# Performance work log

Measured on AMD Instinct MI355X. Metric: run time of the kernel, lower is better.

Reference implementation:

```python
import jax, jax.numpy as jnp
import numpy as np

B, S, D = 2, 1024, 1024
H, HD = 16, 64          # n_heads, head_dim (H*HD == D)
E, FF = 8, 2816         # num_experts, moe hidden_dim
TOP_K = 2               # hard-coded torch.topk(scores, 2)
EPS = 1e-5


def rmsnorm(x, w):
    return x * jax.lax.rsqrt(jnp.mean(x * x, axis=-1, keepdims=True) + EPS) * w


def apply_rope(x, cos, sin):
    # x: [B,S,H,HD]; cos/sin: [S,HD//2] -> interleaved rotary (llama style)
    xr, xi = x[..., 0::2], x[..., 1::2]
    c = cos[None, :, None, :]
    s = sin[None, :, None, :]
    out_r = xr * c - xi * s
    out_i = xr * s + xi * c
    return jnp.stack([out_r, out_i], axis=-1).reshape(x.shape)


def setup_inputs() -> dict:
    key = jax.random.key(0)
    ks = jax.random.split(key, 10)
    sc = 0.02
    pos = jnp.arange(S, dtype=jnp.float32)
    inv = 1.0 / (10000.0 ** (jnp.arange(0, HD, 2, dtype=jnp.float32) / HD))
    ang = pos[:, None] * inv[None, :]                       # [S, HD//2]
    return {
        "x": jax.random.normal(ks[0], (B, S, D), jnp.float32),
        "freqs_cos": jnp.cos(ang),
        "freqs_sin": jnp.sin(ang),
        "attn_norm_w": jnp.ones((D,), jnp.float32),
        "wq": jax.random.normal(ks[1], (D, D), jnp.float32) * sc,
        "wk": jax.random.normal(ks[2], (D, D), jnp.float32) * sc,
        "wv": jax.random.normal(ks[3], (D, D), jnp.float32) * sc,
        "wo": jax.random.normal(ks[4], (D, D), jnp.float32) * sc,
        "ffn_norm_w": jnp.ones((D,), jnp.float32),
        "gate_w": jax.random.normal(ks[5], (E, D), jnp.float32) * sc,
        "w1": jax.random.normal(ks[6], (E, FF, D), jnp.float32) * sc,
        "w2": jax.random.normal(ks[7], (E, FF, D), jnp.float32) * sc,
        "w3": jax.random.normal(ks[8], (E, FF, D), jnp.float32) * sc,
    }


def reference(x, freqs_cos, freqs_sin, attn_norm_w, wq, wk, wv, wo,
              ffn_norm_w, gate_w, w1, w2, w3):
    b, s, d = x.shape

    # ---- pre-norm attention + residual ----
    xn = rmsnorm(x, attn_norm_w)
    q = (xn @ wq.T).reshape(b, s, H, HD)
    k = (xn @ wk.T).reshape(b, s, H, HD)
    v = (xn @ wv.T).reshape(b, s, H, HD)
    q = apply_rope(q, freqs_cos, freqs_sin)
    k = apply_rope(k, freqs_cos, freqs_sin)
    scores = jnp.einsum("bqhd,bkhd->bhqk", q, k) / jnp.sqrt(jnp.float32(HD))
    causal = jnp.tril(jnp.ones((s, s), bool))
    scores = jnp.where(causal[None, None], scores, jnp.finfo(scores.dtype).min)
    attn = jax.nn.softmax(scores, axis=-1)
    o = jnp.einsum("bhqk,bkhd->bqhd", attn, v).reshape(b, s, d) @ wo.T
    h = x + o

    # ---- top-2 MoE FFN (math identical to gather-per-token einsums) ----
    t = rmsnorm(h, ffn_norm_w).reshape(-1, d)               # [T, D]
    T = t.shape[0]
    gate = t @ gate_w.T                                     # [T, E]
    expert_weights, expert_idx = jax.lax.top_k(gate, TOP_K)
    expert_weights = jax.nn.softmax(expert_weights, axis=-1)  # [T, 2]

    x1 = jax.nn.silu(jnp.einsum("td,efd->tef", t, w1))      # [T, E, FF]
    x3 = jnp.einsum("td,efd->tef", t, w3)                   # [T, E, FF]
    ta = jnp.arange(T)[:, None]
    g = x1[ta, expert_idx] * x3[ta, expert_idx]             # [T, 2, FF]
    gw = g * expert_weights[..., None]                      # fold routing weights
    h_full = jnp.zeros((T, E, FF), t.dtype).at[ta, expert_idx].add(gw)
    moe = jnp.einsum("tef,efd->td", h_full, w2)             # [T, D]

    return h + moe.reshape(b, s, d)
```

## Files before the change

kernel.cpp:

```cpp
#include <hip/hip_runtime.h>

#define DI __device__ __forceinline__

typedef __attribute__((ext_vector_type(8))) short short8;
typedef __attribute__((ext_vector_type(4))) float f32x4;

#define DM   1024
#define TT   2048
#define SEQ  1024
#define NHD  16
#define HDD  64
#define NE   8
#define FF   2816

DI ushort f2bf(float f){
  union { float f; unsigned u; } c; c.f = f;
  unsigned u = c.u;
  u += 0x7fffu + ((u >> 16) & 1u);
  return (ushort)(u >> 16);
}
DI float bf2f(ushort b){
  union { unsigned u; float f; } c; c.u = ((unsigned)b) << 16;
  return c.f;
}
DI unsigned pk2(float a, float b){ return (unsigned)f2bf(a) | ((unsigned)f2bf(b) << 16); }
DI uint2 mku2(unsigned a, unsigned b){ uint2 r; r.x = a; r.y = b; return r; }

DI f32x4 MFMA(short8 a, short8 b, f32x4 c){
  return __builtin_amdgcn_mfma_f32_16x16x32_bf16(a, b, c, 0, 0, 0);
}

DI void gload16(const void* g, void* l){
  __builtin_amdgcn_global_load_lds(
      (const __attribute__((address_space(1))) unsigned*)g,
      (__attribute__((address_space(3))) unsigned*)l, 16, 0, 0);
}

#define LDSWZB(row, p) (((row) * 128) + ((((p) ^ ((row) & 7))) * 16))

__global__ __launch_bounds__(256) void k_rmsnorm(const float* __restrict__ x,
                                                 const float* __restrict__ w,
                                                 ushort* __restrict__ xh,
                                                 ushort* __restrict__ xl)
{
  int row = blockIdx.x, tid = threadIdx.x;
  float4 v = ((const float4*)(x + (size_t)row * DM))[tid];
  float ss = v.x*v.x + v.y*v.y + v.z*v.z + v.w*v.w;
#pragma unroll
  for (int m = 32; m >= 1; m >>= 1) ss += __shfl_xor(ss, m);
  __shared__ float sh[4];
  if ((tid & 63) == 0) sh[tid >> 6] = ss;
  __syncthreads();
  ss = sh[0] + sh[1] + sh[2] + sh[3];
  float rstd = 1.0f / sqrtf(ss * (1.0f / DM) + 1e-5f);
  float4 wv = ((const float4*)w)[tid];
  float o0 = v.x * rstd * wv.x, o1 = v.y * rstd * wv.y;
  float o2 = v.z * rstd * wv.z, o3 = v.w * rstd * wv.w;
  ushort h0 = f2bf(o0), h1 = f2bf(o1), h2 = f2bf(o2), h3 = f2bf(o3);
  ((uint2*)(xh + (size_t)row * DM))[tid] =
      mku2((unsigned)h0 | ((unsigned)h1 << 16), (unsigned)h2 | ((unsigned)h3 << 16));
  ((uint2*)(xl + (size_t)row * DM))[tid] =
      mku2(pk2(o0 - bf2f(h0), o1 - bf2f(h1)), pk2(o2 - bf2f(h2), o3 - bf2f(h3)));
}

__global__ __launch_bounds__(256) void k_wsplit(
    const float* __restrict__ wq, const float* __restrict__ wk,
    const float* __restrict__ wv, const float* __restrict__ wo,
    ushort* __restrict__ qh, ushort* __restrict__ ql,
    ushort* __restrict__ kh, ushort* __restrict__ kl,
    ushort* __restrict__ vh, ushort* __restrict__ vl,
    ushort* __restrict__ oh, ushort* __restrict__ ol)
{
  int y = blockIdx.y;
  const float* W = y == 0 ? wq : (y == 1 ? wk : (y == 2 ? wv : wo));
  ushort* H = y == 0 ? qh : (y == 1 ? kh : (y == 2 ? vh : oh));
  ushort* L = y == 0 ? ql : (y == 1 ? kl : (y == 2 ? vl : ol));
  int i = blockIdx.x * 256 + threadIdx.x;
  float4 v = ((const float4*)W)[i];
  ushort h0 = f2bf(v.x), h1 = f2bf(v.y), h2 = f2bf(v.z), h3 = f2bf(v.w);
  ((uint2*)H)[i] = mku2((unsigned)h0 | ((unsigned)h1 << 16),
                        (unsigned)h2 | ((unsigned)h3 << 16));
  ((uint2*)L)[i] = mku2(pk2(v.x - bf2f(h0), v.y - bf2f(h1)),
                        pk2(v.z - bf2f(h2), v.w - bf2f(h3)));
}

__global__ __launch_bounds__(256) void k_cw13(const float* __restrict__ w1,
                                              const float* __restrict__ w3,
                                              ushort* __restrict__ w1b,
                                              ushort* __restrict__ w3b)
{
  const float* src = blockIdx.y ? w3 : w1;
  ushort* dst = blockIdx.y ? w3b : w1b;
  const size_t N4 = (size_t)NE * FF * DM / 4;
  for (size_t i = (size_t)blockIdx.x * 256 + threadIdx.x; i < N4;
       i += (size_t)gridDim.x * 256) {
    float4 v = ((const float4*)src)[i];
    ((uint2*)dst)[i] = mku2(pk2(v.x, v.y), pk2(v.z, v.w));
  }
}

__global__ __launch_bounds__(256, 2) void k_gemm_qkv(
    const ushort* __restrict__ xh, const ushort* __restrict__ xl,
    const ushort* __restrict__ wqh, const ushort* __restrict__ wql,
    const ushort* __restrict__ wkh, const ushort* __restrict__ wkl,
    const ushort* __restrict__ wvh, const ushort* __restrict__ wvl,
    const float* __restrict__ fc, const float* __restrict__ fs,
    ushort* __restrict__ qh, ushort* __restrict__ ql,
    ushort* __restrict__ kh, ushort* __restrict__ kl,
    ushort* __restrict__ vh, ushort* __restrict__ vl)
{
  __shared__ __align__(16) char lds[65536];
  char* Ah = lds;          char* Al = lds + 16384;
  char* Bh = lds + 32768;  char* Bl = lds + 49152;
  int bn = blockIdx.x, bm = blockIdx.y;
  int which = bn >> 3, bnn = bn & 7;
  const ushort* WH = which == 0 ? wqh : (which == 1 ? wkh : wvh);
  const ushort* WL = which == 0 ? wql : (which == 1 ? wkl : wvl);
  int tid = threadIdx.x, lane = tid & 63, w = tid >> 6, wr = w >> 1, wc = w & 1;
  int r0 = lane >> 3, pp = lane & 7;
  size_t asrc[4], bsrc[4]; int cdst[4];
#pragma unroll
  for (int i = 0; i < 4; i++) {
    int c = w * 4 + i;
    int row = c * 8 + r0;
    asrc[i] = (size_t)(bm * 128 + row) * DM + (pp ^ r0) * 8;
    bsrc[i] = (size_t)(bnn * 128 + row) * DM + (pp ^ r0) * 8;
    cdst[i] = c * 1024;
  }
  f32x4 acc[4][4] = {};
  for (int kb = 0; kb < DM; kb += 64) {
    __syncthreads();
#pragma unroll
    for (int i = 0; i < 4; i++) {
      gload16(xh + asrc[i] + kb, Ah + cdst[i]);
      gload16(xl + asrc[i] + kb, Al + cdst[i]);
      gload16(WH + bsrc[i] + kb, Bh + cdst[i]);
      gload16(WL + bsrc[i] + kb, Bl + cdst[i]);
    }
    __syncthreads();
#pragma unroll
    for (int kk = 0; kk < 2; kk++) {
      int j = kk * 4 + (lane >> 4);
      short8 ar[4], al[4];
#pragma unroll
      for (int mi = 0; mi < 4; mi++) {
        int row = wr * 64 + mi * 16 + (lane & 15);
        ar[mi] = *(const short8*)(Ah + LDSWZB(row, j));
        al[mi] = *(const short8*)(Al + LDSWZB(row, j));
      }
#pragma unroll
      for (int ni = 0; ni < 4; ni++) {
        int n = wc * 64 + ni * 16 + (lane & 15);
        short8 b_h = *(const short8*)(Bh + LDSWZB(n, j));
        short8 b_l = *(const short8*)(Bl + LDSWZB(n, j));
#pragma unroll
        for (int mi = 0; mi < 4; mi++) {
          acc[mi][ni] = MFMA(ar[mi], b_h, acc[mi][ni]);
          acc[mi][ni] = MFMA(al[mi], b_h, acc[mi][ni]);
          acc[mi][ni] = MFMA(ar[mi], b_l, acc[mi][ni]);
        }
      }
    }
  }
  ushort* OH = which == 0 ? qh : kh;
  ushort* OL = which == 0 ? ql : kl;
#pragma unroll
  for (int mi = 0; mi < 4; mi++)
#pragma unroll
    for (int ni = 0; ni < 4; ni++)
#pragma unroll
      for (int r = 0; r < 4; r++) {
        int rg = bm*128 + wr*64 + mi*16 + (lane >> 4)*4 + r;
        int cg = bnn*128 + wc*64 + ni*16 + (lane & 15);
        float v = acc[mi][ni][r];
        int b = rg >> 10, s = rg & 1023, hh = cg >> 6, hd = cg & 63;
        if (which <= 1) {
          float p = __shfl_xor(v, 1);
          int pi = hd >> 1;
          float c = fc[s*32 + pi], sn = fs[s*32 + pi];
          float rr = (hd & 1) ? (p * sn + v * c) : (v * c - p * sn);
          size_t o = ((size_t)(b*NHD + hh) * SEQ + s) * HDD + hd;
          ushort hv = f2bf(rr);
          OH[o] = hv; OL[o] = f2bf(rr - bf2f(hv));
        } else {
          size_t o = ((size_t)((b*NHD + hh)*HDD + hd)) * SEQ + s;
          ushort hv = f2bf(v);
          vh[o] = hv; vl[o] = f2bf(v - bf2f(hv));
        }
      }
}

__global__ __launch_bounds__(256) void k_attn(
    const ushort* __restrict__ qh_, const ushort* __restrict__ ql_,
    const ushort* __restrict__ kh_, const ushort* __restrict__ kl_,
    const ushort* __restrict__ vh_, const ushort* __restrict__ vl_,
    ushort* __restrict__ oh_, ushort* __restrict__ ol_)
{
  __shared__ __align__(16) char KV[32768];
  char* Kh = KV;          char* Kl = KV + 8192;
  char* Vh = KV + 16384;  char* Vl = KV + 24576;
  __shared__ __align__(16) ushort Ph[4*16*64], Pl[4*16*64];
  int qt = blockIdx.x, bh = blockIdx.y;
  int tid = threadIdx.x, lane = tid & 63, w = tid >> 6;
  int r0 = lane >> 3, pp = lane & 7;
  short8 qfh[2], qfl[2];
  int qrow = qt*64 + w*16 + (lane & 15);
#pragma unroll
  for (int ks = 0; ks < 2; ks++) {
    size_t g = ((size_t)bh * SEQ + qrow) * HDD + ks*32 + (lane >> 4)*8;
    qfh[ks] = *(const short8*)(qh_ + g);
    qfl[ks] = *(const short8*)(ql_ + g);
  }
  size_t kbase[2], vbase[2];
#pragma unroll
  for (int i = 0; i < 2; i++) {
    int c = 2*w + i;
    kbase[i] = ((size_t)bh * SEQ + c*8 + r0) * 64 + (pp ^ r0) * 8;
    vbase[i] = ((size_t)bh * 64 + c*8 + r0) * SEQ + (pp ^ r0) * 8;
  }
  f32x4 oacc[4] = {};
  float mrun[4], lrun[4];
#pragma unroll
  for (int r = 0; r < 4; r++) { mrun[r] = -1e30f; lrun[r] = 0.0f; }

  for (int kt = 0; kt <= qt; kt++) {
    __syncthreads();
#pragma unroll
    for (int i = 0; i < 2; i++) {
      int c = 2*w + i;
      size_t ko = kbase[i] + (size_t)kt * 64 * 64;
      size_t vo = vbase[i] + (size_t)kt * 64;
      gload16(kh_ + ko, Kh + c*1024);
      gload16(kl_ + ko, Kl + c*1024);
      gload16(vh_ + vo, Vh + c*1024);
      gload16(vl_ + vo, Vl + c*1024);
    }
    __syncthreads();
    f32x4 sa[4] = {};
#pragma unroll
    for (int j2 = 0; j2 < 4; j2++) {
#pragma unroll
      for (int ks = 0; ks < 2; ks++) {
        int kr = j2*16 + (lane & 15);
        int j = ks*4 + (lane >> 4);
        short8 b_h = *(const short8*)(Kh + LDSWZB(kr, j));
        short8 b_l = *(const short8*)(Kl + LDSWZB(kr, j));
        sa[j2] = MFMA(qfh[ks], b_h, sa[j2]);
        sa[j2] = MFMA(qfl[ks], b_h, sa[j2]);
        sa[j2] = MFMA(qfh[ks], b_l, sa[j2]);
      }
    }
    float sv[4][4];
#pragma unroll
    for (int j2 = 0; j2 < 4; j2++)
#pragma unroll
      for (int r = 0; r < 4; r++) {
        float xx = sa[j2][r] * 0.125f;
        if (kt == qt) {
          int kv = j2*16 + (lane & 15), qi = w*16 + (lane >> 4)*4 + r;
          if (kv > qi) xx = -1e30f;
        }
        sv[j2][r] = xx;
      }
#pragma unroll
    for (int r = 0; r < 4; r++) {
      float mx = fmaxf(fmaxf(sv[0][r], sv[1][r]), fmaxf(sv[2][r], sv[3][r]));
#pragma unroll
      for (int m = 8; m >= 1; m >>= 1) mx = fmaxf(mx, __shfl_xor(mx, m));
      float mn = fmaxf(mrun[r], mx);
      float alp = __expf(mrun[r] - mn);
      mrun[r] = mn;
      float rs = 0.0f;
#pragma unroll
      for (int j2 = 0; j2 < 4; j2++) { float pv = __expf(sv[j2][r] - mn); sv[j2][r] = pv; rs += pv; }
#pragma unroll
      for (int m = 8; m >= 1; m >>= 1) rs += __shfl_xor(rs, m);
      lrun[r] = lrun[r] * alp + rs;
#pragma unroll
      for (int hf = 0; hf < 4; hf++) oacc[hf][r] *= alp;
    }
#pragma unroll
    for (int j2 = 0; j2 < 4; j2++)
#pragma unroll
      for (int r = 0; r < 4; r++) {
        int row = (lane >> 4)*4 + r, col = j2*16 + (lane & 15);
        int d = w*1024 + row*64 + (((col >> 3) ^ (row & 7)) * 8) + (col & 7);
        ushort hv = f2bf(sv[j2][r]);
        Ph[d] = hv; Pl[d] = f2bf(sv[j2][r] - bf2f(hv));
      }
#pragma unroll
    for (int hf = 0; hf < 4; hf++) {
#pragma unroll
      for (int ks = 0; ks < 2; ks++) {
        int prow = lane & 15;
        int j = ks*4 + (lane >> 4);
        int pg = (j ^ (prow & 7)) * 8;
        short8 pfh = *(const short8*)&Ph[w*1024 + prow*64 + pg];
        short8 pfl = *(const short8*)&Pl[w*1024 + prow*64 + pg];
        int vrow = hf*16 + (lane & 15);
        short8 vfh = *(const short8*)(Vh + LDSWZB(vrow, j));
        short8 vfl = *(const short8*)(Vl + LDSWZB(vrow, j));
        oacc[hf] = MFMA(pfh, vfh, oacc[hf]);
        oacc[hf] = MFMA(pfl, vfh, oacc[hf]);
        oacc[hf] = MFMA(pfh, vfl, oacc[hf]);
      }
    }
  }
  int b = bh >> 4, h = bh & 15;
#pragma unroll
  for (int r = 0; r < 4; r++) {
    float li = 1.0f / lrun[r];
    int srow = qt*64 + w*16 + (lane >> 4)*4 + r;
#pragma unroll
    for (int hf = 0; hf < 4; hf++) {
      float v = oacc[hf][r] * li;
      size_t o = ((size_t)(b*SEQ + srow)) * DM + h*HDD + hf*16 + (lane & 15);
      ushort hv = f2bf(v);
      oh_[o] = hv; ol_[o] = f2bf(v - bf2f(hv));
    }
  }
}

__global__ __launch_bounds__(256, 3) void k_gemm_wo(
    const ushort* __restrict__ oh, const ushort* __restrict__ ol,
    const ushort* __restrict__ woh, const ushort* __restrict__ wol,
    const float* __restrict__ x, float* __restrict__ hb)
{
  __shared__ __align__(16) char lds[49152];
  char* Ah = lds;          char* Al = lds + 8192;
  char* Bh = lds + 16384;  char* Bl = lds + 32768;
  int bnn = blockIdx.x, bm = blockIdx.y;
  int tid = threadIdx.x, lane = tid & 63, w = tid >> 6;
  int r0 = lane >> 3, pp = lane & 7;
  size_t asrc[2]; int adst[2];
#pragma unroll
  for (int i = 0; i < 2; i++) {
    int c = w * 2 + i;
    int row = c * 8 + r0;
    asrc[i] = (size_t)(bm * 64 + row) * DM + (pp ^ r0) * 8;
    adst[i] = c * 1024;
  }
  size_t bsrc[4]; int bdst[4];
#pragma unroll
  for (int i = 0; i < 4; i++) {
    int c = w * 4 + i;
    int row = c * 8 + r0;
    bsrc[i] = (size_t)(bnn * 128 + row) * DM + (pp ^ r0) * 8;
    bdst[i] = c * 1024;
  }
  f32x4 acc[4][2] = {};
  for (int kb = 0; kb < DM; kb += 64) {
    __syncthreads();
#pragma unroll
    for (int i = 0; i < 2; i++) {
      gload16(oh + asrc[i] + kb, Ah + adst[i]);
      gload16(ol + asrc[i] + kb, Al + adst[i]);
    }
#pragma unroll
    for (int i = 0; i < 4; i++) {
      gload16(woh + bsrc[i] + kb, Bh + bdst[i]);
      gload16(wol + bsrc[i] + kb, Bl + bdst[i]);
    }
    __syncthreads();
#pragma unroll
    for (int kk = 0; kk < 2; kk++) {
      int j = kk * 4 + (lane >> 4);
      short8 ar[4], al[4];
#pragma unroll
      for (int mi = 0; mi < 4; mi++) {
        int row = mi * 16 + (lane & 15);
        ar[mi] = *(const short8*)(Ah + LDSWZB(row, j));
        al[mi] = *(const short8*)(Al + LDSWZB(row, j));
      }
#pragma unroll
      for (int ni = 0; ni < 2; ni++) {
        int n = w * 32 + ni * 16 + (lane & 15);
        short8 b_h = *(const short8*)(Bh + LDSWZB(n, j));
        short8 b_l = *(const short8*)(Bl + LDSWZB(n, j));
#pragma unroll
        for (int mi = 0; mi < 4; mi++) {
          acc[mi][ni] = MFMA(ar[mi], b_h, acc[mi][ni]);
          acc[mi][ni] = MFMA(al[mi], b_h, acc[mi][ni]);
          acc[mi][ni] = MFMA(ar[mi], b_l, acc[mi][ni]);
        }
      }
    }
  }
#pragma unroll
  for (int mi = 0; mi < 4; mi++)
#pragma unroll
    for (int ni = 0; ni < 2; ni++)
#pragma unroll
      for (int r = 0; r < 4; r++) {
        int rg = bm*64 + mi*16 + (lane >> 4)*4 + r;
        int cg = bnn*128 + w*32 + ni*16 + (lane & 15);
        hb[(size_t)rg * DM + cg] = x[(size_t)rg * DM + cg] + acc[mi][ni][r];
      }
}

__global__ __launch_bounds__(256) void k_gate(
    const float* __restrict__ hb, const float* __restrict__ fw, const float* __restrict__ gwt,
    ushort* __restrict__ tb, int* __restrict__ idx, float* __restrict__ ew, int* __restrict__ cnt)
{
  int t = blockIdx.x, tid = threadIdx.x;
  float4 v = ((const float4*)(hb + (size_t)t * DM))[tid];
  float ss = v.x*v.x + v.y*v.y + v.z*v.z + v.w*v.w;
#pragma unroll
  for (int m = 32; m >= 1; m >>= 1) ss += __shfl_xor(ss, m);
  __shared__ float sh[4];
  if ((tid & 63) == 0) sh[tid >> 6] = ss;
  __syncthreads();
  ss = sh[0] + sh[1] + sh[2] + sh[3];
  float rstd = 1.0f / sqrtf(ss * (1.0f / DM) + 1e-5f);
  float4 wv = ((const float4*)fw)[tid];
  float tv0 = v.x*rstd*wv.x, tv1 = v.y*rstd*wv.y, tv2 = v.z*rstd*wv.z, tv3 = v.w*rstd*wv.w;
  ((uint2*)(tb + (size_t)t * DM))[tid] = mku2(pk2(tv0, tv1), pk2(tv2, tv3));
  float ge[8];
#pragma unroll
  for (int e = 0; e < 8; e++) {
    float4 gv = ((const float4*)(gwt + (size_t)e * DM))[tid];
    float s = tv0*gv.x + tv1*gv.y + tv2*gv.z + tv3*gv.w;
#pragma unroll
    for (int m = 32; m >= 1; m >>= 1) s += __shfl_xor(s, m);
    ge[e] = s;
  }
  __shared__ float gsh[4][8];
  if ((tid & 63) == 0) {
#pragma unroll
    for (int e = 0; e < 8; e++) gsh[tid >> 6][e] = ge[e];
  }
  __syncthreads();
  if (tid == 0) {
    float lg[8];
#pragma unroll
    for (int e = 0; e < 8; e++) lg[e] = gsh[0][e] + gsh[1][e] + gsh[2][e] + gsh[3][e];
    int i0 = 0;
    for (int e = 1; e < 8; e++) if (lg[e] > lg[i0]) i0 = e;
    int i1 = (i0 == 0) ? 1 : 0;
    for (int e = 0; e < 8; e++) if (e != i0 && lg[e] > lg[i1]) i1 = e;
    float ex = __expf(lg[i1] - lg[i0]);
    idx[2*t] = i0; idx[2*t+1] = i1;
    ew[2*t] = 1.0f / (1.0f + ex); ew[2*t+1] = ex / (1.0f + ex);
    atomicAdd(&cnt[i0], 1); atomicAdd(&cnt[i1], 1);
  }
}

__global__ void k_offsets(const int* __restrict__ cnt, int* __restrict__ off,
                          int* __restrict__ fil, int* __restrict__ tmap)
{
  if (threadIdx.x == 0 && blockIdx.x == 0) {
    int a = 0, nt = 0;
    for (int e = 0; e < 8; e++) {
      off[e] = a; a += cnt[e]; fil[e] = 0;
      int m = (cnt[e] + 127) >> 7;
      for (int j = 0; j < m; j++) { tmap[1 + nt] = (e << 8) | j; nt++; }
    }
    tmap[0] = nt;
  }
}

__global__ __launch_bounds__(256) void k_scatter(
    const int* __restrict__ idx, const int* __restrict__ off,
    int* __restrict__ fil, int* __restrict__ ent, int* __restrict__ pos)
{
  int t = blockIdx.x * 256 + threadIdx.x;
  if (t < TT) {
#pragma unroll
    for (int k = 0; k < 2; k++) {
      int e = idx[2*t + k];
      int p = atomicAdd(&fil[e], 1);
      int g = off[e] + p;
      ent[g] = 2*t + k;
      pos[2*t + k] = g;
    }
  }
}

__global__ __launch_bounds__(256) void k_tw2(const float* __restrict__ w2, ushort* __restrict__ w2t)
{
  int dt = blockIdx.x, ft = blockIdx.y, e = blockIdx.z;
  __shared__ ushort lt[64*72];
  int tid = threadIdx.x;
#pragma unroll
  for (int i = 0; i < 4; i++) {
    int c = tid + i*256;
    int r = c >> 4, q = c & 15;
    float4 v = *(const float4*)(w2 + ((size_t)e*FF + ft*64 + r) * DM + dt*64 + q*4);
    lt[(q*4+0)*72 + r] = f2bf(v.x);
    lt[(q*4+1)*72 + r] = f2bf(v.y);
    lt[(q*4+2)*72 + r] = f2bf(v.z);
    lt[(q*4+3)*72 + r] = f2bf(v.w);
  }
  __syncthreads();
#pragma unroll
  for (int i = 0; i < 2; i++) {
    int c = tid + i*256;
    int d = c >> 3, fq = c & 7;
    *(uint4*)(w2t + ((size_t)e*DM + dt*64 + d) * FF + ft*64 + fq*8) = *(const uint4*)&lt[d*72 + fq*8];
  }
}

__global__ __launch_bounds__(256, 4) void k_moe13(
    const ushort* __restrict__ tb, const ushort* __restrict__ w1b, const ushort* __restrict__ w3b,
    const int* __restrict__ ent, const float* __restrict__ ew,
    const int* __restrict__ cnt, const int* __restrict__ off, const int* __restrict__ tmap,
    ushort* __restrict__ gb)
{
  int y = blockIdx.y;
  if (y >= tmap[0]) return;
  int tm = tmap[1 + y];
  int e = tm >> 8, mt = tm & 255;
  int nt = blockIdx.x;
  int cn = cnt[e], oe = off[e];
  __shared__ __align__(16) char lds[32768];
  char* Ab = lds;
  char* B1 = lds + 16384;
  char* B3 = lds + 24576;
  int tid = threadIdx.x, lane = tid & 63, w = tid >> 6;
  int wr = w >> 1, wc = w & 1;
  int r0 = lane >> 3, pp = lane & 7;

  const ushort* abase = tb + (pp ^ r0) * 8;
  unsigned aoff[4];
#pragma unroll
  for (int i = 0; i < 4; i++) {
    int c = w * 4 + i;
    int r = c * 8 + r0;
    int g = oe + mt * 128 + r; if (g > 2*TT - 1) g = 2*TT - 1;
    aoff[i] = (unsigned)((ent[g] >> 1) * DM);
  }
  size_t bofs[2];
#pragma unroll
  for (int i = 0; i < 2; i++) {
    int c = 2 * w + i;
    bofs[i] = ((size_t)e * FF + nt * 64 + c * 8 + r0) * DM + (pp ^ r0) * 8;
  }

  f32x4 acc1[4][2] = {}, acc3[4][2] = {};

  for (int kb = 0; kb < DM; kb += 64) {
    __syncthreads();
#pragma unroll
    for (int i = 0; i < 4; i++)
      gload16(abase + aoff[i] + kb, Ab + (w * 4 + i) * 1024);
#pragma unroll
    for (int i = 0; i < 2; i++) {
      gload16(w1b + bofs[i] + kb, B1 + (2 * w + i) * 1024);
      gload16(w3b + bofs[i] + kb, B3 + (2 * w + i) * 1024);
    }
    __syncthreads();
#pragma unroll
    for (int kk = 0; kk < 2; kk++) {
      int j = kk * 4 + (lane >> 4);
      short8 af[4];
#pragma unroll
      for (int mi = 0; mi < 4; mi++) {
        int row = wr * 64 + mi * 16 + (lane & 15);
        af[mi] = *(const short8*)(Ab + LDSWZB(row, j));
      }
#pragma unroll
      for (int ni = 0; ni < 2; ni++) {
        int n = wc * 32 + ni * 16 + (lane & 15);
        short8 b1f = *(const short8*)(B1 + LDSWZB(n, j));
        short8 b3f = *(const short8*)(B3 + LDSWZB(n, j));
#pragma unroll
        for (int mi = 0; mi < 4; mi++) {
          acc1[mi][ni] = MFMA(af[mi], b1f, acc1[mi][ni]);
          acc3[mi][ni] = MFMA(af[mi], b3f, acc3[mi][ni]);
        }
      }
    }
  }
#pragma unroll
  for (int mi = 0; mi < 4; mi++)
#pragma unroll
    for (int ni = 0; ni < 2; ni++)
#pragma unroll
      for (int r = 0; r < 4; r++) {
        int grow = mt * 128 + wr * 64 + mi * 16 + (lane >> 4) * 4 + r;
        if (grow < cn) {
          int g = oe + grow;
          float gwv = ew[ent[g]];
          int f = nt * 64 + wc * 32 + ni * 16 + (lane & 15);
          float x1 = acc1[mi][ni][r], x3 = acc3[mi][ni][r];
          float sg = x1 / (1.0f + __expf(-x1));
          gb[(size_t)g * FF + f] = f2bf(sg * x3 * gwv);
        }
      }
}

__global__ __launch_bounds__(256, 4) void k_moe2(
    const ushort* __restrict__ gb, const ushort* __restrict__ w2t,
    const int* __restrict__ cnt, const int* __restrict__ off, const int* __restrict__ tmap,
    float* __restrict__ mr)
{
  int y = blockIdx.y;
  if (y >= tmap[0]) return;
  int tm = tmap[1 + y];
  int e = tm >> 8, mt = tm & 255;
  int nt = blockIdx.x;
  int cn = cnt[e], oe = off[e];
  __shared__ __align__(16) char lds[24576];
  char* Ab = lds; char* Bb = lds + 16384;
  int tid = threadIdx.x, lane = tid & 63, w = tid >> 6;
  int r0 = lane >> 3, pp = lane & 7;

  const ushort* abase = gb + (pp ^ r0) * 8;
  unsigned aoff[4];
#pragma unroll
  for (int i = 0; i < 4; i++) {
    int c = w * 4 + i;
    int r = c * 8 + r0;
    int g = oe + mt * 128 + r; if (g > 2*TT - 1) g = 2*TT - 1;
    aoff[i] = (unsigned)(g * FF);
  }
  size_t bofs[2];
#pragma unroll
  for (int i = 0; i < 2; i++) {
    int c = 2 * w + i;
    bofs[i] = ((size_t)e * DM + nt * 64 + c * 8 + r0) * FF + (pp ^ r0) * 8;
  }

  f32x4 a2[2][4] = {};
  for (int kb = 0; kb < FF; kb += 64) {
    __syncthreads();
#pragma unroll
    for (int i = 0; i < 4; i++)
      gload16(abase + aoff[i] + kb, Ab + (w * 4 + i) * 1024);
#pragma unroll
    for (int i = 0; i < 2; i++)
      gload16(w2t + bofs[i] + kb, Bb + (2 * w + i) * 1024);
    __syncthreads();
#pragma unroll
    for (int kk = 0; kk < 2; kk++) {
      int j = kk * 4 + (lane >> 4);
      short8 af[2], bf[4];
#pragma unroll
      for (int mi = 0; mi < 2; mi++) {
        int row = w * 32 + mi * 16 + (lane & 15);
        af[mi] = *(const short8*)(Ab + LDSWZB(row, j));
      }
#pragma unroll
      for (int ni = 0; ni < 4; ni++) {
        int n = ni * 16 + (lane & 15);
        bf[ni] = *(const short8*)(Bb + LDSWZB(n, j));
      }
#pragma unroll
      for (int ni = 0; ni < 4; ni++)
#pragma unroll
        for (int mi = 0; mi < 2; mi++)
          a2[mi][ni] = MFMA(af[mi], bf[ni], a2[mi][ni]);
    }
  }
#pragma unroll
  for (int mi = 0; mi < 2; mi++)
#pragma unroll
    for (int ni = 0; ni < 4; ni++)
#pragma unroll
      for (int r = 0; r < 4; r++) {
        int grow = mt * 128 + w * 32 + mi * 16 + (lane >> 4) * 4 + r;
        if (grow < cn) {
          int cg = nt * 64 + ni * 16 + (lane & 15);
          mr[(size_t)(oe + grow) * DM + cg] = a2[mi][ni][r];
        }
      }
}

__global__ __launch_bounds__(256) void k_final(
    const float* __restrict__ hb, const float* __restrict__ mr,
    const int* __restrict__ pos, float* __restrict__ out)
{
  int t = blockIdx.x, tid = threadIdx.x;
  int g0 = pos[2*t], g1 = pos[2*t+1];
  float4 a  = ((const float4*)(hb + (size_t)t * DM))[tid];
  float4 m0 = ((const float4*)(mr + (size_t)g0 * DM))[tid];
  float4 m1 = ((const float4*)(mr + (size_t)g1 * DM))[tid];
  float4 o;
  o.x = a.x + m0.x + m1.x; o.y = a.y + m0.y + m1.y;
  o.z = a.z + m0.z + m1.z; o.w = a.w + m0.w + m1.w;
  ((float4*)(out + (size_t)t * DM))[tid] = o;
}

extern "C" void kernel_launch(void* const* d_in, const int* in_sizes, int n_in,
                              void* d_out, int out_size, void* d_ws, size_t ws_size,
                              hipStream_t stream)
{
  const float* x   = (const float*)d_in[0];
  const float* fc  = (const float*)d_in[1];
  const float* fs  = (const float*)d_in[2];
  const float* anw = (const float*)d_in[3];
  const float* wq  = (const float*)d_in[4];
  const float* wk  = (const float*)d_in[5];
  const float* wv  = (const float*)d_in[6];
  const float* wo  = (const float*)d_in[7];
  const float* fnw = (const float*)d_in[8];
  const float* gwm = (const float*)d_in[9];
  const float* w1  = (const float*)d_in[10];
  const float* w2  = (const float*)d_in[11];
  const float* w3  = (const float*)d_in[12];
  float* out = (float*)d_out;

  char* p = (char*)d_ws;
  auto alloc = [&](size_t n) { char* r = p; p += (n + 255) & ~(size_t)255; return r; };
  ushort* xnh = (ushort*)alloc((size_t)TT*DM*2);
  ushort* xnl = (ushort*)alloc((size_t)TT*DM*2);
  char*   pad = alloc((size_t)TT*DM*8);
  ushort* qh  = (ushort*)alloc((size_t)TT*DM*2);
  ushort* ql  = (ushort*)alloc((size_t)TT*DM*2);
  ushort* kh  = (ushort*)alloc((size_t)TT*DM*2);
  ushort* kl  = (ushort*)alloc((size_t)TT*DM*2);
  ushort* vh  = (ushort*)alloc((size_t)TT*DM*2);
  ushort* vl  = (ushort*)alloc((size_t)TT*DM*2);
  ushort* oh  = (ushort*)alloc((size_t)TT*DM*2);
  ushort* ol  = (ushort*)alloc((size_t)TT*DM*2);
  float*  hb  = (float*) alloc((size_t)TT*DM*4);
  ushort* tb  = (ushort*)alloc((size_t)TT*DM*2);
  ushort* w2t = (ushort*)alloc((size_t)NE*FF*DM*2);
  ushort* gb  = (ushort*)alloc((size_t)2*TT*FF*2);
  float*  mr  = (float*) alloc((size_t)2*TT*DM*4);
  int*    idx = (int*)   alloc((size_t)2*TT*4);
  float*  ew  = (float*) alloc((size_t)2*TT*4);
  int*    ent = (int*)   alloc((size_t)2*TT*4);
  int*    pos = (int*)   alloc((size_t)2*TT*4);
  int*    cnt = (int*)   alloc(32);
  int*    off = (int*)   alloc(32);
  int*    fil = (int*)   alloc(32);
  int*    tmap= (int*)   alloc(256);
  (void)pad;

  ushort* wsp = (ushort*)mr;
  const size_t WN = (size_t)DM * DM;
  ushort* wqh = wsp;        ushort* wql = wsp + WN;
  ushort* wkh = wsp + 2*WN; ushort* wkl = wsp + 3*WN;
  ushort* wvh = wsp + 4*WN; ushort* wvl = wsp + 5*WN;
  ushort* woh = wsp + 6*WN; ushort* wol = wsp + 7*WN;

  ushort* w1b = (ushort*)d_ws;
  ushort* w3b = (ushort*)alloc((size_t)NE*FF*DM*2);

  hipMemsetAsync(cnt, 0, 32, stream);
  k_rmsnorm<<<TT, 256, 0, stream>>>(x, anw, xnh, xnl);
  k_wsplit<<<dim3(1024, 4), 256, 0, stream>>>(wq, wk, wv, wo,
      wqh, wql, wkh, wkl, wvh, wvl, woh, wol);
  k_tw2<<<dim3(16, 44, 8), 256, 0, stream>>>(w2, w2t);
  k_gemm_qkv<<<dim3(24, 16), 256, 0, stream>>>(xnh, xnl,
      wqh, wql, wkh, wkl, wvh, wvl, fc, fs, qh, ql, kh, kl, vh, vl);
  k_attn<<<dim3(16, 32), 256, 0, stream>>>(qh, ql, kh, kl, vh, vl, oh, ol);
  k_gemm_wo<<<dim3(8, 32), 256, 0, stream>>>(oh, ol, woh, wol, x, hb);
  k_gate<<<TT, 256, 0, stream>>>(hb, fnw, gwm, tb, idx, ew, cnt);
  k_offsets<<<1, 64, 0, stream>>>(cnt, off, fil, tmap);
  k_scatter<<<8, 256, 0, stream>>>(idx, off, fil, ent, pos);
  k_cw13<<<dim3(2048, 2), 256, 0, stream>>>(w1, w3, w1b, w3b);
  k_moe13<<<dim3(44, 48), 256, 0, stream>>>(tb, w1b, w3b, ent, ew, cnt, off, tmap, gb);
  k_moe2<<<dim3(16, 48), 256, 0, stream>>>(gb, w2t, cnt, off, tmap, mr);
  k_final<<<TT, 256, 0, stream>>>(hb, mr, pos, out);
  (void)in_sizes; (void)n_in; (void)out_size; (void)ws_size;
}
```

Baseline: 438.4 us.

## Fuse weight conversion and w2 transpose into attention kernel as extra blocks

Attention, the w1/w3 bf16 conversion and the w2 transpose are merged into one launch, with extra blocks beyond the attention grid doing the weight preprocessing. The aim is to overlap the memory-bound conversion with the compute-bound attention and to remove separate launches. This needs a fresh w1b buffer so the conversion no longer aliases workspace still in use, and it falls back to the old path when the workspace is too small. Attention LDS is now carved from one 48KB shared buffer used by all block types, which may affect occupancy.

```diff
diff --git a/kernel.cpp b/kernel.cpp
--- a/kernel.cpp
+++ b/kernel.cpp
@@ -96,6 +96,30 @@
        i += (size_t)gridDim.x * 256) {
     float4 v = ((const float4*)src)[i];
     ((uint2*)dst)[i] = mku2(pk2(v.x, v.y), pk2(v.z, v.w));
+  }
+}
+
+__global__ __launch_bounds__(256) void k_tw2(const float* __restrict__ w2, ushort* __restrict__ w2t)
+{
+  int dt = blockIdx.x, ft = blockIdx.y, e = blockIdx.z;
+  __shared__ ushort lt[64*72];
+  int tid = threadIdx.x;
+#pragma unroll
+  for (int i = 0; i < 4; i++) {
+    int c = tid + i*256;
+    int r = c >> 4, q = c & 15;
+    float4 v = *(const float4*)(w2 + ((size_t)e*FF + ft*64 + r) * DM + dt*64 + q*4);
+    lt[(q*4+0)*72 + r] = f2bf(v.x);
+    lt[(q*4+1)*72 + r] = f2bf(v.y);
+    lt[(q*4+2)*72 + r] = f2bf(v.z);
+    lt[(q*4+3)*72 + r] = f2bf(v.w);
+  }
+  __syncthreads();
+#pragma unroll
+  for (int i = 0; i < 2; i++) {
+    int c = tid + i*256;
+    int d = c >> 3, fq = c & 7;
+    *(uint4*)(w2t + ((size_t)e*DM + dt*64 + d) * FF + ft*64 + fq*8) = *(const uint4*)&lt[d*72 + fq*8];
   }
 }
 
@@ -190,18 +214,64 @@
       }
 }
 
-__global__ __launch_bounds__(256) void k_attn(
+__global__ __launch_bounds__(256) void k_attn_prep(
     const ushort* __restrict__ qh_, const ushort* __restrict__ ql_,
     const ushort* __restrict__ kh_, const ushort* __restrict__ kl_,
     const ushort* __restrict__ vh_, const ushort* __restrict__ vl_,
-    ushort* __restrict__ oh_, ushort* __restrict__ ol_)
-{
-  __shared__ __align__(16) char KV[32768];
-  char* Kh = KV;          char* Kl = KV + 8192;
-  char* Vh = KV + 16384;  char* Vl = KV + 24576;
-  __shared__ __align__(16) ushort Ph[4*16*64], Pl[4*16*64];
-  int qt = blockIdx.x, bh = blockIdx.y;
-  int tid = threadIdx.x, lane = tid & 63, w = tid >> 6;
+    ushort* __restrict__ oh_, ushort* __restrict__ ol_,
+    const float* __restrict__ w1, const float* __restrict__ w3,
+    ushort* __restrict__ w1b, ushort* __restrict__ w3b,
+    const float* __restrict__ w2, ushort* __restrict__ w2t)
+{
+  __shared__ __align__(16) char smem[49152];
+  int bid = blockIdx.x, tid = threadIdx.x;
+
+  if (bid >= 1024) {
+    ushort* lt = (ushort*)smem;
+    int pid = bid - 1024;
+    for (int tt = pid; tt < 16*44*8; tt += 512) {
+      int dt = tt & 15, rest = tt >> 4;
+      int ft = rest % 44, e = rest / 44;
+#pragma unroll
+      for (int i = 0; i < 4; i++) {
+        int c = tid + i*256;
+        int r = c >> 4, q = c & 15;
+        float4 v = *(const float4*)(w2 + ((size_t)e*FF + ft*64 + r) * DM + dt*64 + q*4);
+        lt[(q*4+0)*72 + r] = f2bf(v.x);
+        lt[(q*4+1)*72 + r] = f2bf(v.y);
+        lt[(q*4+2)*72 + r] = f2bf(v.z);
+        lt[(q*4+3)*72 + r] = f2bf(v.w);
+      }
+      __syncthreads();
+#pragma unroll
+      for (int i = 0; i < 2; i++) {
+        int c = tid + i*256;
+        int d = c >> 3, fq = c & 7;
+        *(uint4*)(w2t + ((size_t)e*DM + dt*64 + d) * FF + ft*64 + fq*8) =
+            *(const uint4*)&lt[d*72 + fq*8];
+      }
+      __syncthreads();
+    }
+    return;
+  }
+  if (bid >= 512) {
+    int pid = bid - 512;
+    const size_t N4 = (size_t)NE * FF * DM / 4;
+    for (size_t i = (size_t)pid * 256 + tid; i < N4; i += (size_t)512 * 256) {
+      float4 v = ((const float4*)w1)[i];
+      ((uint2*)w1b)[i] = mku2(pk2(v.x, v.y), pk2(v.z, v.w));
+      float4 u = ((const float4*)w3)[i];
+      ((uint2*)w3b)[i] = mku2(pk2(u.x, u.y), pk2(u.z, u.w));
+    }
+    return;
+  }
+
+  char* Kh = smem;          char* Kl = smem + 8192;
+  char* Vh = smem + 16384;  char* Vl = smem + 24576;
+  ushort* Ph = (ushort*)(smem + 32768);
+  ushort* Pl = (ushort*)(smem + 40960);
+  int qt = bid & 15, bh = bid >> 4;
+  int lane = tid & 63, w = tid >> 6;
   int r0 = lane >> 3, pp = lane & 7;
   short8 qfh[2], qfl[2];
   int qrow = qt*64 + w*16 + (lane & 15);
@@ -473,30 +543,6 @@
       ent[g] = 2*t + k;
       pos[2*t + k] = g;
     }
-  }
-}
-
-__global__ __launch_bounds__(256) void k_tw2(const float* __restrict__ w2, ushort* __restrict__ w2t)
-{
-  int dt = blockIdx.x, ft = blockIdx.y, e = blockIdx.z;
-  __shared__ ushort lt[64*72];
-  int tid = threadIdx.x;
-#pragma unroll
-  for (int i = 0; i < 4; i++) {
-    int c = tid + i*256;
-    int r = c >> 4, q = c & 15;
-    float4 v = *(const float4*)(w2 + ((size_t)e*FF + ft*64 + r) * DM + dt*64 + q*4);
-    lt[(q*4+0)*72 + r] = f2bf(v.x);
-    lt[(q*4+1)*72 + r] = f2bf(v.y);
-    lt[(q*4+2)*72 + r] = f2bf(v.z);
-    lt[(q*4+3)*72 + r] = f2bf(v.w);
-  }
-  __syncthreads();
-#pragma unroll
-  for (int i = 0; i < 2; i++) {
-    int c = tid + i*256;
-    int d = c >> 3, fq = c & 7;
-    *(uint4*)(w2t + ((size_t)e*DM + dt*64 + d) * FF + ft*64 + fq*8) = *(const uint4*)&lt[d*72 + fq*8];
   }
 }
 
@@ -704,7 +750,7 @@
   auto alloc = [&](size_t n) { char* r = p; p += (n + 255) & ~(size_t)255; return r; };
   ushort* xnh = (ushort*)alloc((size_t)TT*DM*2);
   ushort* xnl = (ushort*)alloc((size_t)TT*DM*2);
-  char*   pad = alloc((size_t)TT*DM*8);
+  char*   pad = alloc((size_t)8*1024*1024);
   ushort* qh  = (ushort*)alloc((size_t)TT*DM*2);
   ushort* ql  = (ushort*)alloc((size_t)TT*DM*2);
   ushort* kh  = (ushort*)alloc((size_t)TT*DM*2);
@@ -735,24 +781,34 @@
   ushort* wvh = wsp + 4*WN; ushort* wvl = wsp + 5*WN;
   ushort* woh = wsp + 6*WN; ushort* wol = wsp + 7*WN;
 
-  ushort* w1b = (ushort*)d_ws;
   ushort* w3b = (ushort*)alloc((size_t)NE*FF*DM*2);
+  ushort* w1b_fresh = (ushort*)alloc((size_t)NE*FF*DM*2);
+  bool big = ((size_t)(p - (char*)d_ws) <= ws_size);
+  ushort* w1b = big ? w1b_fresh : (ushort*)d_ws;
 
   hipMemsetAsync(cnt, 0, 32, stream);
   k_rmsnorm<<<TT, 256, 0, stream>>>(x, anw, xnh, xnl);
   k_wsplit<<<dim3(1024, 4), 256, 0, stream>>>(wq, wk, wv, wo,
       wqh, wql, wkh, wkl, wvh, wvl, woh, wol);
-  k_tw2<<<dim3(16, 44, 8), 256, 0, stream>>>(w2, w2t);
   k_gemm_qkv<<<dim3(24, 16), 256, 0, stream>>>(xnh, xnl,
       wqh, wql, wkh, wkl, wvh, wvl, fc, fs, qh, ql, kh, kl, vh, vl);
-  k_attn<<<dim3(16, 32), 256, 0, stream>>>(qh, ql, kh, kl, vh, vl, oh, ol);
+  if (big) {
+    k_attn_prep<<<1536, 256, 0, stream>>>(qh, ql, kh, kl, vh, vl, oh, ol,
+        w1, w3, w1b, w3b, w2, w2t);
+  } else {
+    k_tw2<<<dim3(16, 44, 8), 256, 0, stream>>>(w2, w2t);
+    k_attn_prep<<<512, 256, 0, stream>>>(qh, ql, kh, kl, vh, vl, oh, ol,
+        w1, w3, w1b, w3b, w2, w2t);
+  }
   k_gemm_wo<<<dim3(8, 32), 256, 0, stream>>>(oh, ol, woh, wol, x, hb);
   k_gate<<<TT, 256, 0, stream>>>(hb, fnw, gwm, tb, idx, ew, cnt);
   k_offsets<<<1, 64, 0, stream>>>(cnt, off, fil, tmap);
   k_scatter<<<8, 256, 0, stream>>>(idx, off, fil, ent, pos);
-  k_cw13<<<dim3(2048, 2), 256, 0, stream>>>(w1, w3, w1b, w3b);
+  if (!big) {
+    k_cw13<<<dim3(2048, 2), 256, 0, stream>>>(w1, w3, w1b, w3b);
+  }
   k_moe13<<<dim3(44, 48), 256, 0, stream>>>(tb, w1b, w3b, ent, ew, cnt, off, tmap, gb);
   k_moe2<<<dim3(16, 48), 256, 0, stream>>>(gb, w2t, cnt, off, tmap, mr);
   k_final<<<TT, 256, 0, stream>>>(hb, mr, pos, out);
-  (void)in_sizes; (void)n_in; (void)out_size; (void)ws_size;
-}
+  (void)in_sizes; (void)n_in; (void)out_size;
+}
```

Result: faster. 418.8 us (-4.5%).
